# Performance work log

Hardware: AMD Instinct MI355X
Metric: run time of the kernel (lower is better)

The kernel has to match this reference:

```python
import jax, jax.numpy as jnp
import numpy as np

N = 100000   # num_nodes
E = 600000   # num_edges (before self loops)
H = 128      # hidden_size
R = 16       # lora_rank
SCALING = 32.0 / 16  # lora_alpha / lora_rank
LN_EPS = 1e-5


def setup_inputs() -> dict:
    key = jax.random.key(0)
    ks = jax.random.split(key, 12)
    s = 0.02
    return {
        "hidden_states": jax.random.normal(ks[0], (N, H), dtype=jnp.float32),
        "edge_index": jax.random.randint(ks[1], (2, E), 0, N, dtype=jnp.int64),
        # message_transform (LoRALinear): base W/b + lora A/B
        "msg_W": jax.random.normal(ks[2], (H, H), dtype=jnp.float32) * s,
        "msg_b": jax.random.normal(ks[3], (H,), dtype=jnp.float32) * s,
        "msg_A": jax.random.normal(ks[4], (R, H), dtype=jnp.float32) * s,
        "msg_B": jax.random.normal(ks[5], (H, R), dtype=jnp.float32) * s,
        # gate_transform (LoRALinear)
        "gate_W": jax.random.normal(ks[6], (H, H), dtype=jnp.float32) * s,
        "gate_b": jax.random.normal(ks[7], (H,), dtype=jnp.float32) * s,
        "gate_A": jax.random.normal(ks[8], (R, H), dtype=jnp.float32) * s,
        "gate_B": jax.random.normal(ks[9], (H, R), dtype=jnp.float32) * s,
        # LayerNorm params
        "ln_gamma": jnp.ones((H,), dtype=jnp.float32),
        "ln_beta": jnp.zeros((H,), dtype=jnp.float32),
    }


def _lora_linear(x, W, b, A, B):
    # base_layer(x) + scaling * lora_B(lora_A(x)); dropout is identity at eval
    return x @ W.T + b + SCALING * ((x @ A.T) @ B.T)


def _message_passing(x, edge_index):
    n = x.shape[0]
    loops = jnp.arange(n, dtype=edge_index.dtype)
    row = jnp.concatenate([edge_index[0], loops])  # sources j
    col = jnp.concatenate([edge_index[1], loops])  # targets i
    # symmetric-ish norm: deg from targets (PyG degree(col))
    deg = jax.ops.segment_sum(jnp.ones_like(col, dtype=x.dtype), col, num_segments=n)
    dinv = jnp.where(deg > 0, deg ** -0.5, 0.0)
    norm = dinv[row] * dinv[col]                   # [E+N]
    msgs = norm[:, None] * x[row]                  # edge-gathered messages
    summed = jax.ops.segment_sum(msgs, col, num_segments=n)
    # aggr='mean': divide by per-target edge count (== deg, includes self loop)
    return summed / jnp.maximum(deg, 1.0)[:, None]


def reference(hidden_states, edge_index, msg_W, msg_b, msg_A, msg_B,
              gate_W, gate_b, gate_A, gate_B, ln_gamma, ln_beta):
    message_out = _message_passing(hidden_states, edge_index)
    message_transformed = _lora_linear(message_out, msg_W, msg_b, msg_A, msg_B)
    gate = jax.nn.sigmoid(_lora_linear(hidden_states, gate_W, gate_b, gate_A, gate_B))
    x = hidden_states + gate * message_transformed
    mu = jnp.mean(x, axis=-1, keepdims=True)
    var = jnp.mean(jnp.square(x - mu), axis=-1, keepdims=True)
    return (x - mu) / jnp.sqrt(var + LN_EPS) * ln_gamma + ln_beta
```

## Files before the change

### kernel.cpp

```cpp
#include <hip/hip_runtime.h>
#include <math.h>

#define H 128
#define RANK 16
#define SCALING 2.0f
#define LN_EPS 1e-5f
#define PAD 48

typedef short bf16x8 __attribute__((ext_vector_type(8)));
typedef float f32x4 __attribute__((ext_vector_type(4)));

__device__ __forceinline__ unsigned short f2bf(float f) {
    unsigned int u = __float_as_uint(f);
    u += 0x7fffu + ((u >> 16) & 1u);
    return (unsigned short)(u >> 16);
}
__device__ __forceinline__ unsigned int pk2(float a, float b) {
    return (unsigned int)f2bf(a) | ((unsigned int)f2bf(b) << 16);
}
__device__ __forceinline__ float bflo(unsigned int u) {
    return __uint_as_float(u << 16);
}
__device__ __forceinline__ float bfhi(unsigned int u) {
    return __uint_as_float(u & 0xffff0000u);
}

__global__ __launch_bounds__(256) void k_init(
    const int* __restrict__ ei, int E,
    int* __restrict__ deg, int* __restrict__ adj,
    const float4* __restrict__ x4, int total16, unsigned int* __restrict__ xb,
    const float* __restrict__ msg_W, const float* __restrict__ msg_A,
    const float* __restrict__ msg_B,
    const float* __restrict__ gate_W, const float* __restrict__ gate_A,
    const float* __restrict__ gate_B,
    unsigned short* __restrict__ Wmz, unsigned short* __restrict__ Wgz,
    int BA, int BB) {
    int b = blockIdx.x;
    int t = threadIdx.x;
    if (b < BA) {
        int q = b * 256 + t;
        int e0 = q * 4;
        if ((E & 3) == 0) {
            if (e0 < E) {
                int4 cv = ((const int4*)(ei + E))[q];
                int4 sv = ((const int4*)ei)[q];
                int cc[4] = {cv.x, cv.y, cv.z, cv.w};
                int ss[4] = {sv.x, sv.y, sv.z, sv.w};
                #pragma unroll
                for (int j = 0; j < 4; ++j) {
                    int pos = atomicAdd(&deg[cc[j]], 1);
                    if (pos < PAD) adj[cc[j] * PAD + pos] = ss[j];
                }
            }
        } else {
            #pragma unroll
            for (int j = 0; j < 4; ++j) {
                int e = e0 + j;
                if (e < E) {
                    int c = ei[E + e];
                    int pos = atomicAdd(&deg[c], 1);
                    if (pos < PAD) adj[c * PAD + pos] = ei[e];
                }
            }
        }
    } else if (b < BA + BB) {
        int idx = (b - BA) * 256 + t;
        if (idx < total16) {
            float4 a = x4[idx * 4 + 0];
            float4 bq = x4[idx * 4 + 1];
            float4 cq = x4[idx * 4 + 2];
            float4 dq = x4[idx * 4 + 3];
            uint4 o0, o1;
            o0.x = pk2(a.x, a.y);   o0.y = pk2(a.z, a.w);
            o0.z = pk2(bq.x, bq.y); o0.w = pk2(bq.z, bq.w);
            o1.x = pk2(cq.x, cq.y); o1.y = pk2(cq.z, cq.w);
            o1.z = pk2(dq.x, dq.y); o1.w = pk2(dq.z, dq.w);
            uint4* xb4 = (uint4*)xb;
            xb4[idx * 2 + 0] = o0;
            xb4[idx * 2 + 1] = o1;
        }
    } else {
        int bb = b - BA - BB;
        int which = bb >> 6;
        int idx = (bb & 63) * 256 + t;
        const float* W = which ? gate_W : msg_W;
        const float* A = which ? gate_A : msg_A;
        const float* Bm = which ? gate_B : msg_B;
        unsigned short* Wz = which ? Wgz : Wmz;
        int h = idx & (H - 1);
        int k = idx >> 7;
        float s = 0.f;
        #pragma unroll
        for (int r = 0; r < RANK; ++r) s = fmaf(A[r * H + k], Bm[h * RANK + r], s);
        float v = W[h * H + k] + SCALING * s;
        int kt = k >> 5, kk = k & 31, qd = kk >> 3, j = kk & 7;
        int nt = h >> 4, nl = h & 15;
        int lane = qd * 16 + nl;
        Wz[(((kt * 8 + nt) * 64 + lane) * 8) + j] = f2bf(v);
    }
}

__global__ __launch_bounds__(256) void k_gather(
    const unsigned int* __restrict__ xb, const int* __restrict__ adj,
    const int* __restrict__ deg, int N, unsigned int* __restrict__ msgb) {
    int wave = (blockIdx.x * 256 + threadIdx.x) >> 6;
    int lane = threadIdx.x & 63;
    if (wave >= N) return;
    int i = __builtin_amdgcn_readfirstlane(wave);
    int dg = __builtin_amdgcn_readfirstlane(deg[i]);
    float dif = (float)(dg + 1);
    float di = rsqrtf(dif);
    unsigned int su = xb[(size_t)i * 64 + lane];
    float ax[8], ay[8];
    ax[0] = bflo(su) * di; ay[0] = bfhi(su) * di;
    #pragma unroll
    for (int j = 1; j < 8; ++j) { ax[j] = 0.f; ay[j] = 0.f; }
    int cnt = dg < PAD ? dg : PAD;
    int s0 = i * PAD, s1 = s0 + cnt;
    int last = s1 - 1;
    for (int e = s0; e < s1; e += 8) {
        int is[8]; float ws[8]; unsigned int us[8];
        #pragma unroll
        for (int j = 0; j < 8; ++j) {
            int ee = e + j;
            is[j] = __builtin_amdgcn_readfirstlane(adj[ee < s1 ? ee : last]);
        }
        #pragma unroll
        for (int j = 0; j < 8; ++j) {
            float w = rsqrtf((float)(deg[is[j]] + 1));
            ws[j] = (e + j < s1) ? w : 0.f;
        }
        #pragma unroll
        for (int j = 0; j < 8; ++j) us[j] = xb[(size_t)is[j] * 64 + lane];
        #pragma unroll
        for (int j = 0; j < 8; ++j) {
            ax[j] = fmaf(ws[j], bflo(us[j]), ax[j]);
            ay[j] = fmaf(ws[j], bfhi(us[j]), ay[j]);
        }
    }
    float sc = di / dif;
    float rx = (((ax[0] + ax[1]) + (ax[2] + ax[3])) + ((ax[4] + ax[5]) + (ax[6] + ax[7]))) * sc;
    float ry = (((ay[0] + ay[1]) + (ay[2] + ay[3])) + ((ay[4] + ay[5]) + (ay[6] + ay[7]))) * sc;
    msgb[(size_t)i * 64 + lane] = (unsigned int)f2bf(rx) | ((unsigned int)f2bf(ry) << 16);
}

__global__ __launch_bounds__(256) void k_fused(
    const unsigned int* __restrict__ xb, const unsigned int* __restrict__ msgb,
    const unsigned short* __restrict__ Wmz, const unsigned short* __restrict__ Wgz,
    const float* __restrict__ msg_b, const float* __restrict__ gate_b,
    const float* __restrict__ gamma, const float* __restrict__ beta,
    float* __restrict__ out, int N) {
    int t = threadIdx.x;
    int wid = t >> 6, lane = t & 63;
    int m0 = (blockIdx.x * 4 + wid) * 16;
    if (m0 >= N) return;

    int quad = lane >> 4;
    int nl = lane & 15;

    int arow = m0 + nl; if (arow >= N) arow = N - 1;
    const bf16x8* hb8 = (const bf16x8*)xb + (size_t)arow * 16;
    const bf16x8* mb8 = (const bf16x8*)msgb + (size_t)arow * 16;

    f32x4 accg[8], accm[8];
    #pragma unroll
    for (int nt = 0; nt < 8; ++nt) {
        accg[nt] = (f32x4)(0.f);
        accm[nt] = (f32x4)(0.f);
    }

    #pragma unroll
    for (int kt = 0; kt < 4; ++kt) {
        bf16x8 ah = hb8[kt * 4 + quad];
        bf16x8 am = mb8[kt * 4 + quad];
        const bf16x8* bg8 = (const bf16x8*)(Wgz + (size_t)kt * 4096);
        const bf16x8* bm8 = (const bf16x8*)(Wmz + (size_t)kt * 4096);
        #pragma unroll
        for (int nt = 0; nt < 8; ++nt) {
            bf16x8 bg = bg8[nt * 64 + lane];
            bf16x8 bm = bm8[nt * 64 + lane];
            accg[nt] = __builtin_amdgcn_mfma_f32_16x16x32_bf16(ah, bg, accg[nt], 0, 0, 0);
            accm[nt] = __builtin_amdgcn_mfma_f32_16x16x32_bf16(am, bm, accm[nt], 0, 0, 0);
        }
    }

    float gb[8], mb[8], gm[8], bt[8];
    #pragma unroll
    for (int nt = 0; nt < 8; ++nt) {
        int col = nt * 16 + nl;
        gb[nt] = gate_b[col]; mb[nt] = msg_b[col];
        gm[nt] = gamma[col];  bt[nt] = beta[col];
    }

    const unsigned short* xs = (const unsigned short*)xb;

    #pragma unroll
    for (int r = 0; r < 4; ++r) {
        int node = m0 + quad * 4 + r;
        int hnode = node < N ? node : N - 1;
        const unsigned short* hrow = xs + (size_t)hnode * H;
        float xr[8]; float s = 0.f, ss = 0.f;
        #pragma unroll
        for (int nt = 0; nt < 8; ++nt) {
            int col = nt * 16 + nl;
            float hv = __uint_as_float((unsigned int)hrow[col] << 16);
            float g = 1.f / (1.f + __expf(-(accg[nt][r] + gb[nt])));
            float m = accm[nt][r] + mb[nt];
            float v = fmaf(g, m, hv);
            xr[nt] = v; s += v; ss = fmaf(v, v, ss);
        }
        #pragma unroll
        for (int msk = 1; msk < 16; msk <<= 1) {
            s += __shfl_xor(s, msk);
            ss += __shfl_xor(ss, msk);
        }
        float mu = s * (1.f / 128.f);
        float var = ss * (1.f / 128.f) - mu * mu;
        float rstd = rsqrtf(var + LN_EPS);
        if (node < N) {
            float* orow = out + (size_t)node * H;
            #pragma unroll
            for (int nt = 0; nt < 8; ++nt)
                orow[nt * 16 + nl] = (xr[nt] - mu) * rstd * gm[nt] + bt[nt];
        }
    }
}

extern "C" void kernel_launch(void* const* d_in, const int* in_sizes, int n_in,
                              void* d_out, int out_size, void* d_ws, size_t ws_size,
                              hipStream_t stream) {
    const float* hidden = (const float*)d_in[0];
    const int*   ei     = (const int*)d_in[1];
    const float* msg_W  = (const float*)d_in[2];
    const float* msg_b  = (const float*)d_in[3];
    const float* msg_A  = (const float*)d_in[4];
    const float* msg_B  = (const float*)d_in[5];
    const float* gate_W = (const float*)d_in[6];
    const float* gate_b = (const float*)d_in[7];
    const float* gate_A = (const float*)d_in[8];
    const float* gate_B = (const float*)d_in[9];
    const float* gamma  = (const float*)d_in[10];
    const float* beta   = (const float*)d_in[11];
    float* out = (float*)d_out;

    int N = in_sizes[0] / H;
    int E = in_sizes[1] / 2;

    char* p = (char*)d_ws;
    unsigned short* Wmz = (unsigned short*)p;  p += (size_t)H * H * sizeof(unsigned short);
    unsigned short* Wgz = (unsigned short*)p;  p += (size_t)H * H * sizeof(unsigned short);
    unsigned int* xb   = (unsigned int*)p;     p += (size_t)N * 64 * sizeof(unsigned int);
    unsigned int* msgb = (unsigned int*)p;     p += (size_t)N * 64 * sizeof(unsigned int);
    int* deg = (int*)p;                        p += (size_t)N * sizeof(int);

    int* adj = (int*)d_out;

    hipMemsetAsync(deg, 0, (size_t)N * sizeof(int), stream);

    int BA = (E + 1023) / 1024;
    int total16 = (N * H) >> 4;
    int BB = (total16 + 255) / 256;

    k_init<<<BA + BB + 128, 256, 0, stream>>>(
        ei, E, deg, adj, (const float4*)hidden, total16, xb,
        msg_W, msg_A, msg_B, gate_W, gate_A, gate_B, Wmz, Wgz, BA, BB);

    k_gather<<<((size_t)N * 64 + 255) / 256, 256, 0, stream>>>(
        xb, adj, deg, N, msgb);

    int waves = (N + 15) / 16;
    k_fused<<<(waves + 3) / 4, 256, 0, stream>>>(
        xb, msgb, Wmz, Wgz, msg_b, gate_b, gamma, beta, out, N);
}
```

Before: 243.0 us.

## Fuse neighbor gather into MFMA epilogue kernel via swizzled LDS staging

Merges the per-node gather kernel into the fused GEMM/LayerNorm kernel. Each wave aggregates its 16 rows sequentially into a swizzled LDS tile, which then feeds the message-side MFMA operand directly. This removes the global msgb round trip and one launch. It also moves the adjacency buffer from the output to the workspace and gives each edge-scatter thread 8 edges with batched atomics. The trade-off is far fewer waves doing the latency-bound gather, 16 rows serially per wave, so memory latency may be exposed more.

```diff
diff --git a/kernel.cpp b/kernel.cpp
--- a/kernel.cpp
+++ b/kernel.cpp
@@ -39,22 +39,25 @@
     int t = threadIdx.x;
     if (b < BA) {
         int q = b * 256 + t;
-        int e0 = q * 4;
-        if ((E & 3) == 0) {
+        int e0 = q * 8;
+        if ((E & 7) == 0) {
             if (e0 < E) {
-                int4 cv = ((const int4*)(ei + E))[q];
-                int4 sv = ((const int4*)ei)[q];
-                int cc[4] = {cv.x, cv.y, cv.z, cv.w};
-                int ss[4] = {sv.x, sv.y, sv.z, sv.w};
+                const int4* colv = (const int4*)(ei + E);
+                const int4* srcv = (const int4*)ei;
+                int4 c0 = colv[q * 2], c1 = colv[q * 2 + 1];
+                int4 s0 = srcv[q * 2], s1 = srcv[q * 2 + 1];
+                int cc[8] = {c0.x, c0.y, c0.z, c0.w, c1.x, c1.y, c1.z, c1.w};
+                int ss[8] = {s0.x, s0.y, s0.z, s0.w, s1.x, s1.y, s1.z, s1.w};
+                int pos[8];
                 #pragma unroll
-                for (int j = 0; j < 4; ++j) {
-                    int pos = atomicAdd(&deg[cc[j]], 1);
-                    if (pos < PAD) adj[cc[j] * PAD + pos] = ss[j];
-                }
+                for (int j = 0; j < 8; ++j) pos[j] = atomicAdd(&deg[cc[j]], 1);
+                #pragma unroll
+                for (int j = 0; j < 8; ++j)
+                    if (pos[j] < PAD) adj[cc[j] * PAD + pos[j]] = ss[j];
             }
         } else {
             #pragma unroll
-            for (int j = 0; j < 4; ++j) {
+            for (int j = 0; j < 8; ++j) {
                 int e = e0 + j;
                 if (e < E) {
                     int c = ei[E + e];
@@ -100,67 +103,67 @@
     }
 }
 
-__global__ __launch_bounds__(256) void k_gather(
+__global__ __launch_bounds__(256) void k_mega(
     const unsigned int* __restrict__ xb, const int* __restrict__ adj,
-    const int* __restrict__ deg, int N, unsigned int* __restrict__ msgb) {
-    int wave = (blockIdx.x * 256 + threadIdx.x) >> 6;
-    int lane = threadIdx.x & 63;
-    if (wave >= N) return;
-    int i = __builtin_amdgcn_readfirstlane(wave);
-    int dg = __builtin_amdgcn_readfirstlane(deg[i]);
-    float dif = (float)(dg + 1);
-    float di = rsqrtf(dif);
-    unsigned int su = xb[(size_t)i * 64 + lane];
-    float ax[8], ay[8];
-    ax[0] = bflo(su) * di; ay[0] = bfhi(su) * di;
-    #pragma unroll
-    for (int j = 1; j < 8; ++j) { ax[j] = 0.f; ay[j] = 0.f; }
-    int cnt = dg < PAD ? dg : PAD;
-    int s0 = i * PAD, s1 = s0 + cnt;
-    int last = s1 - 1;
-    for (int e = s0; e < s1; e += 8) {
-        int is[8]; float ws[8]; unsigned int us[8];
-        #pragma unroll
-        for (int j = 0; j < 8; ++j) {
-            int ee = e + j;
-            is[j] = __builtin_amdgcn_readfirstlane(adj[ee < s1 ? ee : last]);
-        }
-        #pragma unroll
-        for (int j = 0; j < 8; ++j) {
-            float w = rsqrtf((float)(deg[is[j]] + 1));
-            ws[j] = (e + j < s1) ? w : 0.f;
-        }
-        #pragma unroll
-        for (int j = 0; j < 8; ++j) us[j] = xb[(size_t)is[j] * 64 + lane];
-        #pragma unroll
-        for (int j = 0; j < 8; ++j) {
-            ax[j] = fmaf(ws[j], bflo(us[j]), ax[j]);
-            ay[j] = fmaf(ws[j], bfhi(us[j]), ay[j]);
-        }
-    }
-    float sc = di / dif;
-    float rx = (((ax[0] + ax[1]) + (ax[2] + ax[3])) + ((ax[4] + ax[5]) + (ax[6] + ax[7]))) * sc;
-    float ry = (((ay[0] + ay[1]) + (ay[2] + ay[3])) + ((ay[4] + ay[5]) + (ay[6] + ay[7]))) * sc;
-    msgb[(size_t)i * 64 + lane] = (unsigned int)f2bf(rx) | ((unsigned int)f2bf(ry) << 16);
-}
-
-__global__ __launch_bounds__(256) void k_fused(
-    const unsigned int* __restrict__ xb, const unsigned int* __restrict__ msgb,
+    const int* __restrict__ deg,
     const unsigned short* __restrict__ Wmz, const unsigned short* __restrict__ Wgz,
     const float* __restrict__ msg_b, const float* __restrict__ gate_b,
     const float* __restrict__ gamma, const float* __restrict__ beta,
     float* __restrict__ out, int N) {
+    __shared__ unsigned int msgLds[64 * 64];
     int t = threadIdx.x;
     int wid = t >> 6, lane = t & 63;
     int m0 = (blockIdx.x * 4 + wid) * 16;
     if (m0 >= N) return;
 
+    char* rowbase = (char*)(msgLds + wid * 16 * 64);
+
+    for (int r16 = 0; r16 < 16; ++r16) {
+        int i0 = m0 + r16;
+        int i = __builtin_amdgcn_readfirstlane(i0 < N ? i0 : N - 1);
+        int dg = __builtin_amdgcn_readfirstlane(deg[i]);
+        float dif = (float)(dg + 1);
+        float di = rsqrtf(dif);
+        unsigned int su = xb[(size_t)i * 64 + lane];
+        float ax[8], ay[8];
+        ax[0] = bflo(su) * di; ay[0] = bfhi(su) * di;
+        #pragma unroll
+        for (int j = 1; j < 8; ++j) { ax[j] = 0.f; ay[j] = 0.f; }
+        int cnt = dg < PAD ? dg : PAD;
+        int s0 = i * PAD, s1 = s0 + cnt;
+        int last = s1 - 1;
+        for (int e = s0; e < s1; e += 8) {
+            int is[8]; float ws[8]; unsigned int us[8];
+            #pragma unroll
+            for (int j = 0; j < 8; ++j) {
+                int ee = e + j;
+                is[j] = __builtin_amdgcn_readfirstlane(adj[ee < s1 ? ee : last]);
+            }
+            #pragma unroll
+            for (int j = 0; j < 8; ++j) {
+                float w = rsqrtf((float)(deg[is[j]] + 1));
+                ws[j] = (e + j < s1) ? w : 0.f;
+            }
+            #pragma unroll
+            for (int j = 0; j < 8; ++j) us[j] = xb[(size_t)is[j] * 64 + lane];
+            #pragma unroll
+            for (int j = 0; j < 8; ++j) {
+                ax[j] = fmaf(ws[j], bflo(us[j]), ax[j]);
+                ay[j] = fmaf(ws[j], bfhi(us[j]), ay[j]);
+            }
+        }
+        float sc = di / dif;
+        float rx = (((ax[0] + ax[1]) + (ax[2] + ax[3])) + ((ax[4] + ax[5]) + (ax[6] + ax[7]))) * sc;
+        float ry = (((ay[0] + ay[1]) + (ay[2] + ay[3])) + ((ay[4] + ay[5]) + (ay[6] + ay[7]))) * sc;
+        int wbyte = ((r16 * 64 + lane) << 2) ^ ((r16 & 7) << 4);
+        *(unsigned int*)(rowbase + wbyte) = pk2(rx, ry);
+    }
+
     int quad = lane >> 4;
     int nl = lane & 15;
 
     int arow = m0 + nl; if (arow >= N) arow = N - 1;
     const bf16x8* hb8 = (const bf16x8*)xb + (size_t)arow * 16;
-    const bf16x8* mb8 = (const bf16x8*)msgb + (size_t)arow * 16;
 
     f32x4 accg[8], accm[8];
     #pragma unroll
@@ -172,7 +175,8 @@
     #pragma unroll
     for (int kt = 0; kt < 4; ++kt) {
         bf16x8 ah = hb8[kt * 4 + quad];
-        bf16x8 am = mb8[kt * 4 + quad];
+        int rbyte = (nl * 256 + kt * 64 + quad * 16) ^ ((nl & 7) << 4);
+        bf16x8 am = *(const bf16x8*)(rowbase + rbyte);
         const bf16x8* bg8 = (const bf16x8*)(Wgz + (size_t)kt * 4096);
         const bf16x8* bm8 = (const bf16x8*)(Wmz + (size_t)kt * 4096);
         #pragma unroll
@@ -250,14 +254,12 @@
     unsigned short* Wmz = (unsigned short*)p;  p += (size_t)H * H * sizeof(unsigned short);
     unsigned short* Wgz = (unsigned short*)p;  p += (size_t)H * H * sizeof(unsigned short);
     unsigned int* xb   = (unsigned int*)p;     p += (size_t)N * 64 * sizeof(unsigned int);
-    unsigned int* msgb = (unsigned int*)p;     p += (size_t)N * 64 * sizeof(unsigned int);
     int* deg = (int*)p;                        p += (size_t)N * sizeof(int);
-
-    int* adj = (int*)d_out;
+    int* adj = (int*)p;                        p += (size_t)N * PAD * sizeof(int);
 
     hipMemsetAsync(deg, 0, (size_t)N * sizeof(int), stream);
 
-    int BA = (E + 1023) / 1024;
+    int BA = (E + 2047) / 2048;
     int total16 = (N * H) >> 4;
     int BB = (total16 + 255) / 256;
 
@@ -265,10 +267,7 @@
         ei, E, deg, adj, (const float4*)hidden, total16, xb,
         msg_W, msg_A, msg_B, gate_W, gate_A, gate_B, Wmz, Wgz, BA, BB);
 
-    k_gather<<<((size_t)N * 64 + 255) / 256, 256, 0, stream>>>(
-        xb, adj, deg, N, msgb);
-
-    int waves = (N + 15) / 16;
-    k_fused<<<(waves + 3) / 4, 256, 0, stream>>>(
-        xb, msgb, Wmz, Wgz, msg_b, gate_b, gamma, beta, out, N);
-}
+    int mblocks = (N + 63) / 64;
+    k_mega<<<mblocks, 256, 0, stream>>>(
+        xb, adj, deg, Wmz, Wgz, msg_b, gate_b, gamma, beta, out, N);
+}
```

New measurement: 316.3 us. 1.3x slower.
